# Kernel optimization log

Hardware: AMD Instinct MI355X
Metric: run time of the kernel (lower is better)

## Reference

```python
import jax, jax.numpy as jnp
import numpy as np

N = 50000      # nodes
E = 600000     # edges
D = 128        # in_channels
H = 128        # hidden_channels
C = 16         # out_channels
L = 3          # num GIN layers
G = 512        # graphs in batch
BN_EPS = 1e-5


def setup_inputs() -> dict:
    key = jax.random.key(0)
    ks = jax.random.split(key, 18)
    s = 0.05
    x = jax.random.normal(ks[0], (N, D), jnp.float32)
    edge_index = jax.random.randint(ks[1], (2, E), 0, N, dtype=jnp.int32)
    batch = jnp.sort(jax.random.randint(ks[2], (N,), 0, G, dtype=jnp.int32))
    # per-layer GIN MLP params (in_channels == hidden, so layers stack uniformly)
    W1s = jax.random.normal(ks[3], (L, D, H), jnp.float32) * s
    b1s = jnp.zeros((L, H), jnp.float32)
    g1s = jnp.ones((L, H), jnp.float32)    # inner BatchNorm gamma
    be1s = jnp.zeros((L, H), jnp.float32)  # inner BatchNorm beta
    W2s = jax.random.normal(ks[4], (L, H, H), jnp.float32) * s
    b2s = jnp.zeros((L, H), jnp.float32)
    gns = jnp.ones((L, H), jnp.float32)    # outer (post-conv) BatchNorm gamma
    bns = jnp.zeros((L, H), jnp.float32)
    # classifier head
    Wc1 = jax.random.normal(ks[5], (H, H), jnp.float32) * s
    bc1 = jnp.zeros((H,), jnp.float32)
    gc = jnp.ones((H,), jnp.float32)
    bec = jnp.zeros((H,), jnp.float32)
    Wc2 = jax.random.normal(ks[6], (H, C), jnp.float32) * s
    bc2 = jnp.zeros((C,), jnp.float32)
    return dict(x=x, edge_index=edge_index, batch=batch, W1s=W1s, b1s=b1s,
                g1s=g1s, be1s=be1s, W2s=W2s, b2s=b2s, gns=gns, bns=bns,
                Wc1=Wc1, bc1=bc1, gc=gc, bec=bec, Wc2=Wc2, bc2=bc2)


def _bn(h, gamma, beta):
    # BatchNorm1d in training mode: batch statistics over the node/row dim
    m = jnp.mean(h, axis=0)
    v = jnp.mean((h - m) ** 2, axis=0)
    return gamma * (h - m) * jax.lax.rsqrt(v + BN_EPS) + beta


def reference(x, edge_index, batch, W1s, b1s, g1s, be1s, W2s, b2s, gns, bns,
              Wc1, bc1, gc, bec, Wc2, bc2):
    src, dst = edge_index[0], edge_index[1]
    h = x
    for l in range(L):
        # GINConv, eps=0: mlp((1+eps)*x_i + sum_{j->i} x_j)
        agg = jax.ops.segment_sum(h[src], dst, num_segments=N) + h
        z = agg @ W1s[l] + b1s[l]
        z = jax.nn.relu(_bn(z, g1s[l], be1s[l]))
        z = z @ W2s[l] + b2s[l]
        h = jax.nn.relu(_bn(z, gns[l], bns[l]))
    # global mean pool over graphs
    counts = jax.ops.segment_sum(jnp.ones((N,), h.dtype), batch, num_segments=G)
    pooled = jax.ops.segment_sum(h, batch, num_segments=G) / jnp.maximum(counts, 1.0)[:, None]
    z = pooled @ Wc1 + bc1
    z = jax.nn.relu(_bn(z, gc, bec))
    return z @ Wc2 + bc2  # [G, C]
```

## Files before the change

### kernel.cpp

```cpp
#include <hip/hip_runtime.h>
#include <hip/hip_fp16.h>

#define NN 50000
#define NE 600000
#define DIM 128
#define NG 512
#define OC 16
#define BN_EPS 1e-5f

typedef __attribute__((ext_vector_type(8))) short short8v;
typedef __attribute__((ext_vector_type(4))) float f32x4;

__device__ inline unsigned short f2bf(float f) {
    unsigned u = __float_as_uint(f);
    u = u + 0x7FFF + ((u >> 16) & 1);
    return (unsigned short)(u >> 16);
}
__device__ inline float bf2f(unsigned short h) {
    return __uint_as_float(((unsigned)h) << 16);
}
__device__ inline float hbits2f(short s) {
    __half_raw hr; hr.x = (unsigned short)s;
    return __half2float(__half(hr));
}
__device__ inline short f2hbits(float f) {
    __half h = __float2half(f);
    short r;
    __builtin_memcpy(&r, &h, 2);
    return r;
}

__global__ void k_hist(const int* __restrict__ dst, int* __restrict__ deg, int e) {
    int i = blockIdx.x * blockDim.x + threadIdx.x;
    if (i < e) atomicAdd(&deg[dst[i]], 1);
}

__global__ void k_scan1(const int* __restrict__ deg, int* __restrict__ pre,
                        int* __restrict__ bsum, int n) {
    __shared__ int lds[1024];
    int t = threadIdx.x;
    int i = blockIdx.x * 1024 + t;
    int v = (i < n) ? deg[i] : 0;
    lds[t] = v;
    __syncthreads();
#pragma unroll
    for (int off = 1; off < 1024; off <<= 1) {
        int add = (t >= off) ? lds[t - off] : 0;
        __syncthreads();
        lds[t] += add;
        __syncthreads();
    }
    if (i < n) pre[i] = lds[t] - v;
    if (t == 1023) bsum[blockIdx.x] = lds[1023];
}

__global__ void k_scan2(int* __restrict__ bsum, int nb) {
    int t = threadIdx.x;
    int v = (t < nb) ? bsum[t] : 0;
    int orig = v;
#pragma unroll
    for (int off = 1; off < 64; off <<= 1) {
        int u = __shfl_up(v, off);
        if (t >= off) v += u;
    }
    if (t < nb) bsum[t] = v - orig;
}

__global__ void k_scan3(const int* __restrict__ pre, const int* __restrict__ bsum,
                        int* __restrict__ row_start, int* __restrict__ cursor, int n) {
    int i = blockIdx.x * blockDim.x + threadIdx.x;
    if (i < n) {
        int r = pre[i] + bsum[i >> 10];
        row_start[i] = r;
        cursor[i] = r;
    }
    if (i == 0) row_start[n] = NE;
}

__global__ void k_scatter(const int* __restrict__ src, const int* __restrict__ dst,
                          int* __restrict__ cursor, int* __restrict__ col, int e) {
    int i = blockIdx.x * blockDim.x + threadIdx.x;
    if (i < e) {
        int d = dst[i];
        int p = atomicAdd(&cursor[d], 1);
        col[p] = src[i];
    }
}

__global__ void k_gstart(const int* __restrict__ batch, int* __restrict__ gstart, int n) {
    int i = blockIdx.x * blockDim.x + threadIdx.x;
    if (i >= n) return;
    int b = batch[i];
    int bp = (i == 0) ? -1 : batch[i - 1];
    for (int g = bp + 1; g <= b; g++) gstart[g] = i;
    if (i == n - 1) {
        for (int g = b + 1; g <= NG; g++) gstart[g] = n;
    }
}

__global__ void k_transform0(const float* __restrict__ in, __half* __restrict__ out, int n4) {
    int i = blockIdx.x * blockDim.x + threadIdx.x;
    if (i >= n4) return;
    float4 v = ((const float4*)in)[i];
    __half2 o0 = __floats2half2_rn(v.x, v.y);
    __half2 o1 = __floats2half2_rn(v.z, v.w);
    uint2 pk;
    pk.x = *(unsigned*)&o0;
    pk.y = *(unsigned*)&o1;
    ((uint2*)out)[i] = pk;
}

template <int TRANSFORM>
__global__ void k_aggregate_q(const __half* __restrict__ Ht, const int* __restrict__ rs,
                              const int* __restrict__ col,
                              const float* __restrict__ stats, const float* __restrict__ gamma,
                              const float* __restrict__ beta, float invn,
                              __half* __restrict__ out, int n) {
    __shared__ float sst[256];
    int tid = threadIdx.x;
    if (TRANSFORM && tid < 128) {
        float s = stats[tid], q = stats[128 + tid];
        float m = s * invn;
        float var = fmaxf(q * invn - m * m, 0.f);
        float r = rsqrtf(var + BN_EPS);
        float sc = gamma[tid] * r;
        sst[tid] = sc;
        sst[128 + tid] = beta[tid] - m * sc;
    }
    if (TRANSFORM) __syncthreads();

    int node = blockIdx.x * 16 + (tid >> 4);
    if (node >= n) return;
    int ql = tid & 15;
    int c = ql * 8;
    float sc[8], sh[8];
    if (TRANSFORM) {
#pragma unroll
        for (int j = 0; j < 8; j++) { sc[j] = sst[c + j]; sh[j] = sst[128 + c + j]; }
    }

    const short8v* Hp = (const short8v*)Ht;
    float acc[8];
    short8v hv = Hp[(size_t)node * 16 + ql];
#pragma unroll
    for (int j = 0; j < 8; j++) {
        float f = hbits2f(hv[j]);
        if (TRANSFORM) f = fmaxf(fmaf(f, sc[j], sh[j]), 0.f);
        acc[j] = f;
    }
    int s = rs[node], e = rs[node + 1];
    int i = s;
    for (; i + 1 < e; i += 2) {
        int j0 = col[i], j1 = col[i + 1];
        short8v u0 = Hp[(size_t)j0 * 16 + ql];
        short8v u1 = Hp[(size_t)j1 * 16 + ql];
#pragma unroll
        for (int j = 0; j < 8; j++) {
            float f0 = hbits2f(u0[j]);
            float f1 = hbits2f(u1[j]);
            if (TRANSFORM) {
                f0 = fmaxf(fmaf(f0, sc[j], sh[j]), 0.f);
                f1 = fmaxf(fmaf(f1, sc[j], sh[j]), 0.f);
            }
            acc[j] += f0 + f1;
        }
    }
    if (i < e) {
        short8v u0 = Hp[(size_t)col[i] * 16 + ql];
#pragma unroll
        for (int j = 0; j < 8; j++) {
            float f0 = hbits2f(u0[j]);
            if (TRANSFORM) f0 = fmaxf(fmaf(f0, sc[j], sh[j]), 0.f);
            acc[j] += f0;
        }
    }
    short8v o;
#pragma unroll
    for (int j = 0; j < 8; j++) o[j] = f2hbits(acc[j]);
    ((short8v*)out)[(size_t)node * 16 + ql] = o;
}

__global__ void k_prepw(const float* __restrict__ W1s, const float* __restrict__ W2s,
                        const float* __restrict__ Wc1, unsigned short* __restrict__ wfrag) {
    int idx = blockIdx.x * blockDim.x + threadIdx.x;
    if (idx >= 7 * 8 * 4 * 64) return;
    int lane = idx & 63;
    int k0 = (idx >> 6) & 3;
    int ct = (idx >> 8) & 7;
    int m = idx >> 11;
    const float* Wsrc = (m < 3) ? (W1s + (size_t)m * 16384)
                      : (m < 6) ? (W2s + (size_t)(m - 3) * 16384)
                                : Wc1;
    int colc = ct * 16 + (lane & 15);
    int kbase = k0 * 32 + (lane >> 4) * 8;
    short8v hi, lo;
#pragma unroll
    for (int j = 0; j < 8; j++) {
        float w = Wsrc[(size_t)(kbase + j) * 128 + colc];
        unsigned short h = f2bf(w);
        hi[j] = (short)h;
        lo[j] = (short)f2bf(w - bf2f(h));
    }
    size_t fo = ((size_t)(ct * 4 + k0) * 64 + lane) * 8;
    *(short8v*)(wfrag + (size_t)(m * 2 + 0) * 16384 + fo) = hi;
    *(short8v*)(wfrag + (size_t)(m * 2 + 1) * 16384 + fo) = lo;
}

#define MFMA(A8, B8, C4) __builtin_amdgcn_mfma_f32_16x16x32_bf16(A8, B8, C4, 0, 0, 0)

#define STORE_STATS(ACT, ACC0, ACC1, SUB)                                          \
    if (ACT) {                                                                     \
        int rowb = (SUB) * 16 + kb * 4;                                            \
        _Pragma("unroll")                                                          \
        for (int j = 0; j < 4; j++) {                                              \
            size_t i0 = (size_t)(rowb + j) * 128 + ct0 * 16 + rlo;                 \
            size_t i1 = (size_t)(rowb + j) * 128 + ct1 * 16 + rlo;                 \
            if (ZHALF) {                                                           \
                ((__half*)Zout)[i0] = __float2half(ACC0[j]);                       \
                ((__half*)Zout)[i1] = __float2half(ACC1[j]);                       \
            } else {                                                               \
                ((float*)Zout)[i0] = ACC0[j];                                      \
                ((float*)Zout)[i1] = ACC1[j];                                      \
            }                                                                      \
        }                                                                          \
        float s0 = ACC0[0] + ACC0[1] + ACC0[2] + ACC0[3];                          \
        float q0 = ACC0[0]*ACC0[0] + ACC0[1]*ACC0[1] + ACC0[2]*ACC0[2] + ACC0[3]*ACC0[3]; \
        float s1 = ACC1[0] + ACC1[1] + ACC1[2] + ACC1[3];                          \
        float q1 = ACC1[0]*ACC1[0] + ACC1[1]*ACC1[1] + ACC1[2]*ACC1[2] + ACC1[3]*ACC1[3]; \
        s0 += __shfl_xor(s0, 16); s0 += __shfl_xor(s0, 32);                        \
        q0 += __shfl_xor(q0, 16); q0 += __shfl_xor(q0, 32);                        \
        s1 += __shfl_xor(s1, 16); s1 += __shfl_xor(s1, 32);                        \
        q1 += __shfl_xor(q1, 16); q1 += __shfl_xor(q1, 32);                        \
        if (kb == 0) {                                                             \
            atomicAdd(&sred[ct0 * 16 + rlo], s0);                                  \
            atomicAdd(&sred[128 + ct0 * 16 + rlo], q0);                            \
            atomicAdd(&sred[ct1 * 16 + rlo], s1);                                  \
            atomicAdd(&sred[128 + ct1 * 16 + rlo], q1);                            \
        }                                                                          \
    }

template <int TRANSFORM, int ZHALF>
__global__ __launch_bounds__(256) void k_gemm_mfma(
        const __half* __restrict__ A, const unsigned short* __restrict__ wfragm,
        const float* __restrict__ bias,
        const float* __restrict__ statsIn, const float* __restrict__ gamma,
        const float* __restrict__ beta, float invn,
        void* __restrict__ Zout, float* __restrict__ statsOut, int nsub) {
    __shared__ short8v wldsHi[1024];
    __shared__ short8v wldsLo[1024];
    __shared__ float sred[256];
    __shared__ float sst[256];
    int tid = threadIdx.x;
    int wid = tid >> 6, lane = tid & 63;
    int sub0 = (blockIdx.x * 4 + wid) * 2;
    bool act0 = sub0 < nsub, act1 = sub0 + 1 < nsub;
    int rlo = lane & 15, kb = lane >> 4;

    sred[tid] = 0.f;
    if (TRANSFORM && tid < 128) {
        float s = statsIn[tid], q = statsIn[128 + tid];
        float m = s * invn;
        float var = fmaxf(q * invn - m * m, 0.f);
        float rs = rsqrtf(var + BN_EPS);
        float sc = gamma[tid] * rs;
        sst[tid] = sc;
        sst[128 + tid] = beta[tid] - m * sc;
    }
    __syncthreads();

    short8v ahi[2][4], alo[2][4];
#pragma unroll
    for (int ss = 0; ss < 2; ss++) {
        bool act = ss ? act1 : act0;
        if (act) {
            const __half* ap = A + ((size_t)(sub0 + ss) * 16 + rlo) * 128;
#pragma unroll
            for (int k0 = 0; k0 < 4; k0++) {
                int c = k0 * 32 + kb * 8;
                short8v hv = *(const short8v*)(ap + c);
#pragma unroll
                for (int j = 0; j < 8; j++) {
                    float f = hbits2f(hv[j]);
                    if (TRANSFORM) f = fmaxf(fmaf(f, sst[c + j], sst[128 + c + j]), 0.f);
                    unsigned short hb = f2bf(f);
                    ahi[ss][k0][j] = (short)hb;
                    alo[ss][k0][j] = (short)f2bf(f - bf2f(hb));
                }
            }
        } else {
#pragma unroll
            for (int k0 = 0; k0 < 4; k0++) {
                ahi[ss][k0] = short8v{0,0,0,0,0,0,0,0};
                alo[ss][k0] = short8v{0,0,0,0,0,0,0,0};
            }
        }
    }

    const float4* wsrc = (const float4*)wfragm;
    float4* dH = (float4*)wldsHi;
    float4* dL = (float4*)wldsLo;

#pragma unroll
    for (int p = 0; p < 2; p++) {
        if (p) __syncthreads();
#pragma unroll
        for (int i = 0; i < 4; i++) {
            dH[tid + 256 * i] = wsrc[p * 1024 + tid + 256 * i];
            dL[tid + 256 * i] = wsrc[2048 + p * 1024 + tid + 256 * i];
        }
        __syncthreads();
#pragma unroll
        for (int cc = 0; cc < 2; cc++) {
            int ctp = 2 * p + cc;
            int ct0 = ctp * 2, ct1 = ct0 + 1;
            int l0 = ct0 - 4 * p, l1 = ct1 - 4 * p;
            float bb0 = bias[ct0 * 16 + rlo], bb1 = bias[ct1 * 16 + rlo];
            f32x4 acc00 = {bb0, bb0, bb0, bb0};
            f32x4 acc01 = {bb1, bb1, bb1, bb1};
            f32x4 acc10 = {bb0, bb0, bb0, bb0};
            f32x4 acc11 = {bb1, bb1, bb1, bb1};
#pragma unroll
            for (int k0 = 0; k0 < 4; k0++) {
                short8v bh0 = wldsHi[(l0 * 4 + k0) * 64 + lane];
                short8v bh1 = wldsHi[(l1 * 4 + k0) * 64 + lane];
                short8v bl0 = wldsLo[(l0 * 4 + k0) * 64 + lane];
                short8v bl1 = wldsLo[(l1 * 4 + k0) * 64 + lane];
                acc00 = MFMA(ahi[0][k0], bh0, acc00);
                acc10 = MFMA(ahi[1][k0], bh0, acc10);
                acc01 = MFMA(ahi[0][k0], bh1, acc01);
                acc11 = MFMA(ahi[1][k0], bh1, acc11);
                acc00 = MFMA(alo[0][k0], bh0, acc00);
                acc10 = MFMA(alo[1][k0], bh0, acc10);
                acc01 = MFMA(alo[0][k0], bh1, acc01);
                acc11 = MFMA(alo[1][k0], bh1, acc11);
                acc00 = MFMA(ahi[0][k0], bl0, acc00);
                acc10 = MFMA(ahi[1][k0], bl0, acc10);
                acc01 = MFMA(ahi[0][k0], bl1, acc01);
                acc11 = MFMA(ahi[1][k0], bl1, acc11);
            }
            STORE_STATS(act0, acc00, acc01, sub0);
            STORE_STATS(act1, acc10, acc11, sub0 + 1);
        }
    }
    __syncthreads();
    if (tid < 128) {
        atomicAdd(&statsOut[tid], sred[tid]);
        atomicAdd(&statsOut[128 + tid], sred[128 + tid]);
    }
}

__global__ void k_pool_seg(const __half* __restrict__ H, const int* __restrict__ gstart,
                           const float* __restrict__ stats, const float* __restrict__ gamma,
                           const float* __restrict__ beta, float invn,
                           __half* __restrict__ out) {
    int g = blockIdx.x;
    int s = gstart[g], e = gstart[g + 1];
    int t = threadIdx.x;
    int lane = t & 63, wave = t >> 6;
    int c0 = lane * 2;
    float sc0, sc1, sh0, sh1;
    {
        float s0 = stats[c0], q0 = stats[128 + c0];
        float m0 = s0 * invn;
        float r0 = rsqrtf(fmaxf(q0 * invn - m0 * m0, 0.f) + BN_EPS);
        sc0 = gamma[c0] * r0; sh0 = beta[c0] - m0 * sc0;
        float s1 = stats[c0 + 1], q1 = stats[129 + c0];
        float m1 = s1 * invn;
        float r1 = rsqrtf(fmaxf(q1 * invn - m1 * m1, 0.f) + BN_EPS);
        sc1 = gamma[c0 + 1] * r1; sh1 = beta[c0 + 1] - m1 * sc1;
    }
    const __half2* Hp = (const __half2*)H;
    float ax = 0.f, ay = 0.f;
    for (int r = s + wave; r < e; r += 4) {
        float2 v = __half22float2(Hp[(size_t)r * 64 + lane]);
        ax += fmaxf(fmaf(v.x, sc0, sh0), 0.f);
        ay += fmaxf(fmaf(v.y, sc1, sh1), 0.f);
    }
    __shared__ float red[2][256];
    red[0][t] = ax;
    red[1][t] = ay;
    __syncthreads();
    if (wave == 0) {
        float inv = 1.f / fmaxf((float)(e - s), 1.f);
        float sx = red[0][lane] + red[0][64 + lane] + red[0][128 + lane] + red[0][192 + lane];
        float sy = red[1][lane] + red[1][64 + lane] + red[1][128 + lane] + red[1][192 + lane];
        ((__half2*)out)[g * 64 + lane] = __floats2half2_rn(sx * inv, sy * inv);
    }
}

__global__ void k_final(const float* __restrict__ Zh, const float* __restrict__ stats,
                        const float* __restrict__ gamma, const float* __restrict__ beta,
                        float invn, const float* __restrict__ Wc2,
                        const float* __restrict__ bc2, float* __restrict__ out) {
    __shared__ float Wl[128 * 16];
    __shared__ float Al[32 * 128];
    int tid = threadIdx.x;
    int kc = tid & 127;
    float s = stats[kc], q = stats[128 + kc];
    float m = s * invn;
    float rs = rsqrtf(fmaxf(q * invn - m * m, 0.f) + BN_EPS);
    float sck = gamma[kc] * rs;
    float shk = beta[kc] - m * sck;
#pragma unroll
    for (int i = 0; i < 4; i++) Wl[tid + 512 * i] = Wc2[tid + 512 * i];
#pragma unroll
    for (int i = 0; i < 8; i++) {
        int idx = tid + 512 * i;
        int gl = idx >> 7, k = idx & 127;
        float a = Zh[(size_t)(blockIdx.x * 32 + gl) * 128 + k];
        Al[idx] = fmaxf(fmaf(a, sck, shk), 0.f);
    }
    __syncthreads();
    int g = tid >> 4, c = tid & 15;
    float acc = bc2[c];
#pragma unroll 8
    for (int k = 0; k < 128; k++) acc = fmaf(Al[g * 128 + k], Wl[k * 16 + c], acc);
    out[(size_t)(blockIdx.x * 32 + g) * 16 + c] = acc;
}

extern "C" void kernel_launch(void* const* d_in, const int* in_sizes, int n_in,
                              void* d_out, int out_size, void* d_ws, size_t ws_size,
                              hipStream_t stream) {
    (void)in_sizes; (void)n_in; (void)out_size; (void)ws_size;
    const float* x    = (const float*)d_in[0];
    const int*   ei   = (const int*)d_in[1];
    const int*   srcv = ei;
    const int*   dstv = ei + NE;
    const int*   batch = (const int*)d_in[2];
    const float* W1s = (const float*)d_in[3];
    const float* b1s = (const float*)d_in[4];
    const float* g1s = (const float*)d_in[5];
    const float* be1s = (const float*)d_in[6];
    const float* W2s = (const float*)d_in[7];
    const float* b2s = (const float*)d_in[8];
    const float* gns = (const float*)d_in[9];
    const float* bns = (const float*)d_in[10];
    const float* Wc1 = (const float*)d_in[11];
    const float* bc1 = (const float*)d_in[12];
    const float* gc  = (const float*)d_in[13];
    const float* bec = (const float*)d_in[14];
    const float* Wc2 = (const float*)d_in[15];
    const float* bc2 = (const float*)d_in[16];
    float* out = (float*)d_out;

    char* ws = (char*)d_ws;
    size_t off = 0;
    auto alloc = [&](size_t bytes) -> char* {
        char* p = ws + off;
        off += (bytes + 255) & ~(size_t)255;
        return p;
    };
    int*   deg     = (int*)alloc(50048 * 4);
    float* statsZ  = (float*)alloc(7 * 256 * 4);
    size_t zeroBytes = off;
    int*   row_start = (int*)alloc((NN + 64) * 4);
    int*   cursor    = (int*)alloc((NN + 64) * 4);
    int*   pre       = (int*)alloc((NN + 64) * 4);
    int*   bsum      = (int*)alloc(64 * 4);
    int*   col       = (int*)alloc((NE + 64) * 4);
    int*   gstart    = (int*)alloc((NG + 1) * 4);
    unsigned short* wfrag = (unsigned short*)alloc((size_t)7 * 2 * 16384 * 2);
    __half* Ht     = (__half*)alloc((size_t)NN * 128 * 2);
    __half* aggH   = (__half*)alloc((size_t)NN * 128 * 2);
    __half* bufBh  = (__half*)alloc((size_t)NN * 128 * 2);
    __half* bufCh  = (__half*)alloc((size_t)NN * 128 * 2);
    __half* headAh = (__half*)alloc((size_t)NG * 128 * 2);
    float*  bufF   = (float*)alloc((size_t)NG * 128 * 4);

    hipMemsetAsync(d_ws, 0, zeroBytes, stream);

    k_prepw<<<56, 256, 0, stream>>>(W1s, W2s, Wc1, wfrag);

    k_hist<<<(NE + 255) / 256, 256, 0, stream>>>(dstv, deg, NE);
    int nb = (NN + 1023) / 1024;
    k_scan1<<<nb, 1024, 0, stream>>>(deg, pre, bsum, NN);
    k_scan2<<<1, 64, 0, stream>>>(bsum, nb);
    k_scan3<<<(NN + 255) / 256, 256, 0, stream>>>(pre, bsum, row_start, cursor, NN);
    k_scatter<<<(NE + 255) / 256, 256, 0, stream>>>(srcv, dstv, cursor, col, NE);
    k_gstart<<<(NN + 255) / 256, 256, 0, stream>>>(batch, gstart, NN);

    int n4 = NN * 32;
    int tGrid = (n4 + 255) / 256;
    int aggGrid = NN / 16;
    int nsub = NN / 16;
    int gGrid = (nsub + 7) / 8;
    float invN = 1.f / NN;

    k_transform0<<<tGrid, 256, 0, stream>>>(x, Ht, n4);

    for (int l = 0; l < 3; l++) {
        float* s1 = statsZ + (size_t)(2 * l) * 256;
        float* s2 = statsZ + (size_t)(2 * l + 1) * 256;
        if (l == 0)
            k_aggregate_q<0><<<aggGrid, 256, 0, stream>>>(
                Ht, row_start, col, nullptr, nullptr, nullptr, 0.f, aggH, NN);
        else
            k_aggregate_q<1><<<aggGrid, 256, 0, stream>>>(
                bufCh, row_start, col, statsZ + (size_t)(2 * l - 1) * 256,
                gns + (l - 1) * 128, bns + (l - 1) * 128, invN, aggH, NN);
        k_gemm_mfma<0, 1><<<gGrid, 256, 0, stream>>>(
            aggH, wfrag + (size_t)(2 * l) * 16384, b1s + l * 128,
            nullptr, nullptr, nullptr, 0.f, bufBh, s1, nsub);
        k_gemm_mfma<1, 1><<<gGrid, 256, 0, stream>>>(
            bufBh, wfrag + (size_t)(2 * (3 + l)) * 16384, b2s + l * 128,
            s1, g1s + l * 128, be1s + l * 128, invN, bufCh, s2, nsub);
    }

    float* s2last = statsZ + (size_t)5 * 256;
    float* sHead  = statsZ + (size_t)6 * 256;
    k_pool_seg<<<NG, 256, 0, stream>>>(bufCh, gstart, s2last, gns + 2 * 128,
                                       bns + 2 * 128, invN, headAh);
    k_gemm_mfma<0, 0><<<4, 256, 0, stream>>>(
        headAh, wfrag + (size_t)12 * 16384, bc1,
        nullptr, nullptr, nullptr, 0.f, bufF, sHead, NG / 16);
    k_final<<<16, 512, 0, stream>>>(bufF, sHead, gc, bec, 1.f / NG, Wc2, bc2, out);
}
```

Before: 341.3 us.

## Fuse neighbor aggregation into first GEMM and merge scan kernels

Replaces the separate aggregation kernel and first MLP GEMM with one kernel. Each block gathers neighbor sums for 64 nodes into shared memory in fp32, then splits them into bf16 hi/lo parts and runs the MFMA GEMM with BN statistics accumulation. This removes the fp16 round trip of the aggregated tensor through global memory and also drops the fp16 rounding of that intermediate. The block-offset scan is folded into k_scan3, so one launch goes away. The cost is heavy shared-memory use (about 48KB per block), which lowers occupancy for the latency-bound gather phase, and the weights are restaged into LDS in every block.

```diff
diff --git a/kernel.cpp b/kernel.cpp
--- a/kernel.cpp
+++ b/kernel.cpp
@@ -54,23 +54,25 @@
     if (t == 1023) bsum[blockIdx.x] = lds[1023];
 }
 
-__global__ void k_scan2(int* __restrict__ bsum, int nb) {
+__global__ void k_scan3(const int* __restrict__ pre, const int* __restrict__ bsum,
+                        int* __restrict__ row_start, int* __restrict__ cursor,
+                        int n, int nb) {
+    __shared__ int boff[64];
     int t = threadIdx.x;
-    int v = (t < nb) ? bsum[t] : 0;
-    int orig = v;
-#pragma unroll
-    for (int off = 1; off < 64; off <<= 1) {
-        int u = __shfl_up(v, off);
-        if (t >= off) v += u;
-    }
-    if (t < nb) bsum[t] = v - orig;
-}
-
-__global__ void k_scan3(const int* __restrict__ pre, const int* __restrict__ bsum,
-                        int* __restrict__ row_start, int* __restrict__ cursor, int n) {
-    int i = blockIdx.x * blockDim.x + threadIdx.x;
+    if (t < 64) {
+        int v = (t < nb) ? bsum[t] : 0;
+        int orig = v;
+#pragma unroll
+        for (int off = 1; off < 64; off <<= 1) {
+            int u = __shfl_up(v, off);
+            if (t >= off) v += u;
+        }
+        boff[t] = v - orig;
+    }
+    __syncthreads();
+    int i = blockIdx.x * blockDim.x + t;
     if (i < n) {
-        int r = pre[i] + bsum[i >> 10];
+        int r = pre[i] + boff[i >> 10];
         row_start[i] = r;
         cursor[i] = r;
     }
@@ -108,76 +110,6 @@
     pk.x = *(unsigned*)&o0;
     pk.y = *(unsigned*)&o1;
     ((uint2*)out)[i] = pk;
-}
-
-template <int TRANSFORM>
-__global__ void k_aggregate_q(const __half* __restrict__ Ht, const int* __restrict__ rs,
-                              const int* __restrict__ col,
-                              const float* __restrict__ stats, const float* __restrict__ gamma,
-                              const float* __restrict__ beta, float invn,
-                              __half* __restrict__ out, int n) {
-    __shared__ float sst[256];
-    int tid = threadIdx.x;
-    if (TRANSFORM && tid < 128) {
-        float s = stats[tid], q = stats[128 + tid];
-        float m = s * invn;
-        float var = fmaxf(q * invn - m * m, 0.f);
-        float r = rsqrtf(var + BN_EPS);
-        float sc = gamma[tid] * r;
-        sst[tid] = sc;
-        sst[128 + tid] = beta[tid] - m * sc;
-    }
-    if (TRANSFORM) __syncthreads();
-
-    int node = blockIdx.x * 16 + (tid >> 4);
-    if (node >= n) return;
-    int ql = tid & 15;
-    int c = ql * 8;
-    float sc[8], sh[8];
-    if (TRANSFORM) {
-#pragma unroll
-        for (int j = 0; j < 8; j++) { sc[j] = sst[c + j]; sh[j] = sst[128 + c + j]; }
-    }
-
-    const short8v* Hp = (const short8v*)Ht;
-    float acc[8];
-    short8v hv = Hp[(size_t)node * 16 + ql];
-#pragma unroll
-    for (int j = 0; j < 8; j++) {
-        float f = hbits2f(hv[j]);
-        if (TRANSFORM) f = fmaxf(fmaf(f, sc[j], sh[j]), 0.f);
-        acc[j] = f;
-    }
-    int s = rs[node], e = rs[node + 1];
-    int i = s;
-    for (; i + 1 < e; i += 2) {
-        int j0 = col[i], j1 = col[i + 1];
-        short8v u0 = Hp[(size_t)j0 * 16 + ql];
-        short8v u1 = Hp[(size_t)j1 * 16 + ql];
-#pragma unroll
-        for (int j = 0; j < 8; j++) {
-            float f0 = hbits2f(u0[j]);
-            float f1 = hbits2f(u1[j]);
-            if (TRANSFORM) {
-                f0 = fmaxf(fmaf(f0, sc[j], sh[j]), 0.f);
-                f1 = fmaxf(fmaf(f1, sc[j], sh[j]), 0.f);
-            }
-            acc[j] += f0 + f1;
-        }
-    }
-    if (i < e) {
-        short8v u0 = Hp[(size_t)col[i] * 16 + ql];
-#pragma unroll
-        for (int j = 0; j < 8; j++) {
-            float f0 = hbits2f(u0[j]);
-            if (TRANSFORM) f0 = fmaxf(fmaf(f0, sc[j], sh[j]), 0.f);
-            acc[j] += f0;
-        }
-    }
-    short8v o;
-#pragma unroll
-    for (int j = 0; j < 8; j++) o[j] = f2hbits(acc[j]);
-    ((short8v*)out)[(size_t)node * 16 + ql] = o;
 }
 
 __global__ void k_prepw(const float* __restrict__ W1s, const float* __restrict__ W2s,
@@ -207,6 +139,153 @@
 }
 
 #define MFMA(A8, B8, C4) __builtin_amdgcn_mfma_f32_16x16x32_bf16(A8, B8, C4, 0, 0, 0)
+
+template <int HASBN>
+__global__ __launch_bounds__(256) void k_agg_gemm(
+        const __half* __restrict__ Ht, const int* __restrict__ rs,
+        const int* __restrict__ colv,
+        const float* __restrict__ stats, const float* __restrict__ gamma,
+        const float* __restrict__ beta, float invn,
+        const unsigned short* __restrict__ wfragm, const float* __restrict__ bias,
+        __half* __restrict__ Zout, float* __restrict__ statsOut,
+        int n, int nsub) {
+    __shared__ float aggL[64 * 128];
+    __shared__ short8v wH[512];
+    __shared__ short8v wL[512];
+    __shared__ float sred[256];
+    __shared__ float sst[256];
+    int tid = threadIdx.x;
+
+    sred[tid] = 0.f;
+    if (HASBN) {
+        if (tid < 128) {
+            float s = stats[tid], q = stats[128 + tid];
+            float m = s * invn;
+            float var = fmaxf(q * invn - m * m, 0.f);
+            float r = rsqrtf(var + BN_EPS);
+            float sc = gamma[tid] * r;
+            sst[tid] = sc;
+            sst[128 + tid] = beta[tid] - m * sc;
+        }
+        __syncthreads();
+    }
+
+    int qw = tid >> 4;
+    int ql = tid & 15;
+    int c = ql * 8;
+    int nodeBase = blockIdx.x * 64;
+    float sc[8], sh[8];
+    if (HASBN) {
+#pragma unroll
+        for (int j = 0; j < 8; j++) { sc[j] = sst[c + j]; sh[j] = sst[128 + c + j]; }
+    }
+    const short8v* Hp = (const short8v*)Ht;
+
+#define TRF(F) (HASBN ? fmaxf(fmaf((F), sc[j], sh[j]), 0.f) : (F))
+#pragma unroll
+    for (int sub = 0; sub < 4; sub++) {
+        int node = nodeBase + sub * 16 + qw;
+        if (node < n) {
+            float acc[8];
+            short8v hv = Hp[(size_t)node * 16 + ql];
+#pragma unroll
+            for (int j = 0; j < 8; j++) { float f = hbits2f(hv[j]); acc[j] = TRF(f); }
+            int s = rs[node], e = rs[node + 1];
+            int i = s;
+            for (; i + 3 < e; i += 4) {
+                int j0 = colv[i], j1 = colv[i + 1], j2 = colv[i + 2], j3 = colv[i + 3];
+                short8v u0 = Hp[(size_t)j0 * 16 + ql];
+                short8v u1 = Hp[(size_t)j1 * 16 + ql];
+                short8v u2 = Hp[(size_t)j2 * 16 + ql];
+                short8v u3 = Hp[(size_t)j3 * 16 + ql];
+#pragma unroll
+                for (int j = 0; j < 8; j++) {
+                    float f0 = hbits2f(u0[j]), f1 = hbits2f(u1[j]);
+                    float f2 = hbits2f(u2[j]), f3 = hbits2f(u3[j]);
+                    acc[j] += TRF(f0) + TRF(f1) + TRF(f2) + TRF(f3);
+                }
+            }
+            for (; i < e; i++) {
+                short8v u0 = Hp[(size_t)colv[i] * 16 + ql];
+#pragma unroll
+                for (int j = 0; j < 8; j++) { float f0 = hbits2f(u0[j]); acc[j] += TRF(f0); }
+            }
+            int lrow = sub * 16 + qw;
+            float4 v0 = make_float4(acc[0], acc[1], acc[2], acc[3]);
+            float4 v1 = make_float4(acc[4], acc[5], acc[6], acc[7]);
+            *(float4*)&aggL[lrow * 128 + c] = v0;
+            *(float4*)&aggL[lrow * 128 + c + 4] = v1;
+        }
+    }
+#undef TRF
+    __syncthreads();
+
+    int wid = tid >> 6, lane = tid & 63;
+    int rlo = lane & 15, kb = lane >> 4;
+    int sub = blockIdx.x * 4 + wid;
+    bool act = sub < nsub;
+
+    short8v ahi[4], alo[4];
+#pragma unroll
+    for (int k0 = 0; k0 < 4; k0++) {
+        const float* ap = &aggL[(wid * 16 + rlo) * 128 + k0 * 32 + kb * 8];
+#pragma unroll
+        for (int j = 0; j < 8; j++) {
+            float f = ap[j];
+            unsigned short hb = f2bf(f);
+            ahi[k0][j] = (short)hb;
+            alo[k0][j] = (short)f2bf(f - bf2f(hb));
+        }
+    }
+
+    const float4* wsrc = (const float4*)wfragm;
+    float4* dH = (float4*)wH;
+    float4* dL = (float4*)wL;
+
+#pragma unroll
+    for (int p = 0; p < 4; p++) {
+        __syncthreads();
+        dH[tid] = wsrc[p * 512 + tid];
+        dH[tid + 256] = wsrc[p * 512 + tid + 256];
+        dL[tid] = wsrc[2048 + p * 512 + tid];
+        dL[tid + 256] = wsrc[2048 + p * 512 + tid + 256];
+        __syncthreads();
+#pragma unroll
+        for (int cc = 0; cc < 2; cc++) {
+            int ct = 2 * p + cc;
+            float bb = bias[ct * 16 + rlo];
+            f32x4 acc = {bb, bb, bb, bb};
+#pragma unroll
+            for (int k0 = 0; k0 < 4; k0++) {
+                short8v bh = wH[(cc * 4 + k0) * 64 + lane];
+                short8v bl = wL[(cc * 4 + k0) * 64 + lane];
+                acc = MFMA(ahi[k0], bh, acc);
+                acc = MFMA(alo[k0], bh, acc);
+                acc = MFMA(ahi[k0], bl, acc);
+            }
+            if (act) {
+#pragma unroll
+                for (int j = 0; j < 4; j++) {
+                    size_t i0 = (size_t)(sub * 16 + kb * 4 + j) * 128 + ct * 16 + rlo;
+                    Zout[i0] = __float2half(acc[j]);
+                }
+                float s0 = acc[0] + acc[1] + acc[2] + acc[3];
+                float q0 = acc[0]*acc[0] + acc[1]*acc[1] + acc[2]*acc[2] + acc[3]*acc[3];
+                s0 += __shfl_xor(s0, 16); s0 += __shfl_xor(s0, 32);
+                q0 += __shfl_xor(q0, 16); q0 += __shfl_xor(q0, 32);
+                if (kb == 0) {
+                    atomicAdd(&sred[ct * 16 + rlo], s0);
+                    atomicAdd(&sred[128 + ct * 16 + rlo], q0);
+                }
+            }
+        }
+    }
+    __syncthreads();
+    if (tid < 128) {
+        atomicAdd(&statsOut[tid], sred[tid]);
+        atomicAdd(&statsOut[128 + tid], sred[128 + tid]);
+    }
+}
 
 #define STORE_STATS(ACT, ACC0, ACC1, SUB)                                          \
     if (ACT) {                                                                     \
@@ -461,7 +540,6 @@
     int*   gstart    = (int*)alloc((NG + 1) * 4);
     unsigned short* wfrag = (unsigned short*)alloc((size_t)7 * 2 * 16384 * 2);
     __half* Ht     = (__half*)alloc((size_t)NN * 128 * 2);
-    __half* aggH   = (__half*)alloc((size_t)NN * 128 * 2);
     __half* bufBh  = (__half*)alloc((size_t)NN * 128 * 2);
     __half* bufCh  = (__half*)alloc((size_t)NN * 128 * 2);
     __half* headAh = (__half*)alloc((size_t)NG * 128 * 2);
@@ -474,15 +552,14 @@
     k_hist<<<(NE + 255) / 256, 256, 0, stream>>>(dstv, deg, NE);
     int nb = (NN + 1023) / 1024;
     k_scan1<<<nb, 1024, 0, stream>>>(deg, pre, bsum, NN);
-    k_scan2<<<1, 64, 0, stream>>>(bsum, nb);
-    k_scan3<<<(NN + 255) / 256, 256, 0, stream>>>(pre, bsum, row_start, cursor, NN);
+    k_scan3<<<(NN + 255) / 256, 256, 0, stream>>>(pre, bsum, row_start, cursor, NN, nb);
     k_scatter<<<(NE + 255) / 256, 256, 0, stream>>>(srcv, dstv, cursor, col, NE);
     k_gstart<<<(NN + 255) / 256, 256, 0, stream>>>(batch, gstart, NN);
 
     int n4 = NN * 32;
     int tGrid = (n4 + 255) / 256;
-    int aggGrid = NN / 16;
     int nsub = NN / 16;
+    int fusedGrid = (NN + 63) / 64;
     int gGrid = (nsub + 7) / 8;
     float invN = 1.f / NN;
 
@@ -492,15 +569,14 @@
         float* s1 = statsZ + (size_t)(2 * l) * 256;
         float* s2 = statsZ + (size_t)(2 * l + 1) * 256;
         if (l == 0)
-            k_aggregate_q<0><<<aggGrid, 256, 0, stream>>>(
-                Ht, row_start, col, nullptr, nullptr, nullptr, 0.f, aggH, NN);
+            k_agg_gemm<0><<<fusedGrid, 256, 0, stream>>>(
+                Ht, row_start, col, nullptr, nullptr, nullptr, 0.f,
+                wfrag + (size_t)(2 * l) * 16384, b1s + l * 128, bufBh, s1, NN, nsub);
         else
-            k_aggregate_q<1><<<aggGrid, 256, 0, stream>>>(
+            k_agg_gemm<1><<<fusedGrid, 256, 0, stream>>>(
                 bufCh, row_start, col, statsZ + (size_t)(2 * l - 1) * 256,
-                gns + (l - 1) * 128, bns + (l - 1) * 128, invN, aggH, NN);
-        k_gemm_mfma<0, 1><<<gGrid, 256, 0, stream>>>(
-            aggH, wfrag + (size_t)(2 * l) * 16384, b1s + l * 128,
-            nullptr, nullptr, nullptr, 0.f, bufBh, s1, nsub);
+                gns + (l - 1) * 128, bns + (l - 1) * 128, invN,
+                wfrag + (size_t)(2 * l) * 16384, b1s + l * 128, bufBh, s1, NN, nsub);
         k_gemm_mfma<1, 1><<<gGrid, 256, 0, stream>>>(
             bufBh, wfrag + (size_t)(2 * (3 + l)) * 16384, b2s + l * 128,
             s1, g1s + l * 128, be1s + l * 128, invN, bufCh, s2, nsub);
```

Result: slower. 399.9 us (+17.2%).
